# Performance work log

Measured on AMD Instinct MI355X. Metric: run time of the kernel, lower is better.

## Reference

```python
import jax, jax.numpy as jnp
import numpy as np

MEM_DIM = 128
ORDER = 256
THETA = 256.0
BATCH = 16
SEQ = 256
IN_DIM = 128


def _lmu_discrete_AB(order, theta):
    # Legendre delay network matrices (same construction as GenerateABMatrix)
    Q = np.arange(order, dtype=np.float64)
    R = (2.0 * Q + 1.0)[:, None]
    j, i = np.meshgrid(Q, Q)
    A = np.where(i < j, -1.0, (-1.0) ** (i - j + 1)) * R          # (O, O)
    B = ((-1.0) ** Q[:, None]) * R                                 # (O, 1)
    At = A.T / theta                                               # transposed system
    Bt = B.T / theta                                               # (1, O)
    # ZOH discretization on the transposed system: expm of padded block matrix
    em = np.concatenate([np.concatenate([At, Bt], axis=0),
                         np.zeros((order + 1, 1))], axis=1)        # (O+1, O+1)
    ms = jax.scipy.linalg.expm(jnp.asarray(em, jnp.float32))
    Ad = ms[:order, :order]                                        # (O, O)
    Bd = ms[order:, :order]                                        # (1, O)
    return Ad, Bd


def setup_inputs() -> dict:
    key = jax.random.key(0)
    kx, kw = jax.random.split(key)
    x = jax.random.normal(kx, (BATCH, SEQ, IN_DIM), dtype=jnp.float32)
    # glorot-uniform MemoryKernel (inputDim, MemoryDim)
    limit = np.sqrt(6.0 / (IN_DIM + MEM_DIM))
    memory_kernel = jax.random.uniform(kw, (IN_DIM, MEM_DIM), dtype=jnp.float32,
                                       minval=-limit, maxval=limit)
    A, B_mat = _lmu_discrete_AB(ORDER, THETA)
    return {"x": x, "memory_kernel": memory_kernel, "A": A, "B_mat": B_mat}


def reference(x, memory_kernel, A, B_mat):
    """LRMUCell (hiddenCell=None, no memory/hidden feedback) unrolled over SEQ.

    Per step: u_t = x_t @ K ; m_t = m_{t-1} @ Ad + u_t[:, :, None] * Bd
    Returns the final flattened memory state (batch, MemoryDim * Order).
    """
    Bsz, T, D = x.shape
    M = memory_kernel.shape[1]
    O = A.shape[0]
    # No feedback into u, so the input projection can be hoisted out of the scan.
    u_all = jnp.einsum('btd,dm->tbm', x, memory_kernel)  # (T, B, M)

    def step(m, u):
        # m: (B, M, O); u: (B, M)
        # (B,M,1) @ (1,O) is an outer product along the last axes
        m_new = jnp.matmul(m, A) + u[..., None] * B_mat
        return m_new, None

    m0 = jnp.zeros((Bsz, M, O), dtype=x.dtype)
    m_final, _ = jax.lax.scan(step, m0, u_all)
    return m_final.reshape(Bsz, M * O)
```

## Files before the change

### kernel.cpp

```cpp
#include <hip/hip_runtime.h>


#define SEQ_T 256
#define DIM 128
#define ORD 256
#define BMROWS 2048
#define NCHAIN 64

#define OFF_U 0
#define OFF_P (SEQ_T * BMROWS)
#define OFF_A0 (OFF_P + ORD * ORD)
#define OFF_A1 (OFF_A0 + ORD * ORD)
#define OFF_FLAGS (OFF_A1 + ORD * ORD)

#define LD_A(p) \
  __hip_atomic_load((p), __ATOMIC_RELAXED, __HIP_MEMORY_SCOPE_AGENT)
#define ST_A(p, v) \
  __hip_atomic_store((p), (v), __ATOMIC_RELAXED, __HIP_MEMORY_SCOPE_AGENT)

__device__ __forceinline__ void chain_bar(unsigned* flags, unsigned target) {
  __syncthreads();
  asm volatile("s_waitcnt vmcnt(0)" ::: "memory");
  const int t = threadIdx.x;
  if (t < NCHAIN) {
    if (t == (int)blockIdx.x) ST_A(&flags[t * 16], target);
    while (LD_A(&flags[t * 16]) < target) __builtin_amdgcn_s_sleep(2);
  }
  __syncthreads();
}

__global__ __launch_bounds__(256) void lrmu_main(
    const float* __restrict__ x, const float* __restrict__ K,
    const float* __restrict__ A, const float* __restrict__ Bm,
    float* __restrict__ ws) {
  __shared__ __align__(16) float ls[6 * ORD];
  __shared__ __align__(16) float red[4 * 6 * ORD];
  float* U = ws + OFF_U;
  float* P = ws + OFF_P;
  float* A0 = ws + OFF_A0;
  float* A1 = ws + OFF_A1;
  unsigned* flags = (unsigned*)(ws + OFF_FLAGS);
  const int blk = blockIdx.x, tid = threadIdx.x;

  if (blk >= NCHAIN) {
    float* xs = red;
    for (int u = blk - NCHAIN; u < 256; u += 256 - NCHAIN) {
      int b = u >> 4, tc = u & 15;
      for (int idx = tid; idx < 16 * DIM; idx += 256)
        xs[idx] = x[(b * SEQ_T + tc * 16) * DIM + idx];
      __syncthreads();
      int m = tid & 127, th = tid >> 7;
      float acc[8] = {};
#pragma unroll 8
      for (int d = 0; d < DIM; ++d) {
        float kv = K[d * DIM + m];
#pragma unroll
        for (int r = 0; r < 8; ++r)
          acc[r] = fmaf(xs[(th * 8 + r) * DIM + d], kv, acc[r]);
      }
#pragma unroll
      for (int r = 0; r < 8; ++r)
        U[(tc * 16 + th * 8 + r) * BMROWS + b * DIM + m] = acc[r];
      __syncthreads();
    }
    return;
  }

  const int lane = tid & 63, q = tid >> 6;
  for (int k = 0; k < 8; ++k) {
    const float* S = (k == 0) ? A : ((k & 1) ? A0 : A1);
    float* Snew = (k & 1) ? A1 : A0;
    const int half = 1 << k;
    const int nsr = (k < 7) ? 4 : 0;
    const int ndr = (k == 7) ? 2 : (blk < half ? 1 : 0);
    const int tr = nsr + ndr;

#pragma unroll
    for (int j = 0; j < 6; ++j) {
      int e = tid + 256 * j;
      int s = e >> 8, c = e & 255;
      float v = 0.f;
      if (s < nsr) {
        v = LD_A((float*)&S[(4 * blk + s) * ORD + c]);
      } else if (s - nsr < ndr) {
        int d = blk + 64 * (s - nsr);
        v = (k == 0) ? Bm[c] : LD_A(&P[d * ORD + c]);
      }
      ls[e] = v;
    }
    if (k == 0 && blk == 0) ST_A(&P[tid], Bm[tid]);
    __syncthreads();

    float acc[6][4];
#pragma unroll
    for (int s = 0; s < 6; ++s)
#pragma unroll
      for (int j = 0; j < 4; ++j) acc[s][j] = 0.f;
#pragma unroll 4
    for (int ii = 0; ii < 64; ++ii) {
      int i = (q << 6) + ii;
      float sv0 = LD_A((float*)&S[i * ORD + lane]);
      float sv1 = LD_A((float*)&S[i * ORD + lane + 64]);
      float sv2 = LD_A((float*)&S[i * ORD + lane + 128]);
      float sv3 = LD_A((float*)&S[i * ORD + lane + 192]);
#pragma unroll
      for (int s = 0; s < 6; ++s) {
        float lv = ls[s * ORD + i];
        acc[s][0] = fmaf(lv, sv0, acc[s][0]);
        acc[s][1] = fmaf(lv, sv1, acc[s][1]);
        acc[s][2] = fmaf(lv, sv2, acc[s][2]);
        acc[s][3] = fmaf(lv, sv3, acc[s][3]);
      }
    }
#pragma unroll
    for (int s = 0; s < 6; ++s)
#pragma unroll
      for (int j = 0; j < 4; ++j)
        red[(q * 6 + s) * ORD + (j << 6) + lane] = acc[s][j];
    __syncthreads();

#pragma unroll
    for (int j = 0; j < 6; ++j) {
      int o = tid + 256 * j;
      int s = o >> 8, c = o & 255;
      if (s < tr) {
        float sum = red[o] + red[1536 + o] + red[3072 + o] + red[4608 + o];
        float* dst;
        if (s < nsr) {
          dst = &Snew[(4 * blk + s) * ORD + c];
        } else {
          int d = blk + 64 * (s - nsr);
          dst = &P[(half + d) * ORD + c];
        }
        ST_A(dst, sum);
      }
    }
    if (k < 7) chain_bar(flags, (unsigned)(k + 1));
  }
}

__global__ __launch_bounds__(256) void lrmu_out(
    const float* __restrict__ U, const float* __restrict__ P,
    float* __restrict__ out) {
  __shared__ __align__(16) float us[SEQ_T * 8];
  int bm0 = blockIdx.x * 8;
  int tid = threadIdx.x;
  for (int idx = tid; idx < SEQ_T * 8; idx += 256) {
    int t = idx >> 3, r = idx & 7;
    us[idx] = U[t * BMROWS + bm0 + r];
  }
  __syncthreads();
  float acc[8] = {};
  int c = tid;
#pragma unroll 8
  for (int t = 0; t < SEQ_T; ++t) {
    float pv = P[(SEQ_T - 1 - t) * ORD + c];
    const float4 u0 = *(const float4*)&us[t * 8];
    const float4 u1 = *(const float4*)&us[t * 8 + 4];
    acc[0] = fmaf(u0.x, pv, acc[0]);
    acc[1] = fmaf(u0.y, pv, acc[1]);
    acc[2] = fmaf(u0.z, pv, acc[2]);
    acc[3] = fmaf(u0.w, pv, acc[3]);
    acc[4] = fmaf(u1.x, pv, acc[4]);
    acc[5] = fmaf(u1.y, pv, acc[5]);
    acc[6] = fmaf(u1.z, pv, acc[6]);
    acc[7] = fmaf(u1.w, pv, acc[7]);
  }
#pragma unroll
  for (int r = 0; r < 8; ++r) out[(bm0 + r) * ORD + c] = acc[r];
}

extern "C" void kernel_launch(void* const* d_in, const int* in_sizes, int n_in,
                              void* d_out, int out_size, void* d_ws,
                              size_t ws_size, hipStream_t stream) {
  const float* x = (const float*)d_in[0];
  const float* K = (const float*)d_in[1];
  const float* A = (const float*)d_in[2];
  const float* Bm = (const float*)d_in[3];
  float* out = (float*)d_out;
  float* ws = (float*)d_ws;

  hipMemsetAsync(ws + OFF_FLAGS, 0, 4096, stream);
  lrmu_main<<<256, 256, 0, stream>>>(x, K, A, Bm, ws);
  lrmu_out<<<BMROWS / 8, 256, 0, stream>>>(ws + OFF_U, ws + OFF_P, out);
}
```

Before: 143.5 us.

## Fuse projection, squaring chain and output into one persistent kernel

Merges the projection, the matrix-power doubling chain and the output contraction into a single 256-block kernel that uses grid-wide flag barriers. The chain work is now split over all 256 blocks as 64 row groups by 4 column groups, with the S column tile staged in LDS and partial sums reduced by shuffles. Each squaring step writes to its own buffer, so there are no read/write hazards across steps. The intent is to remove a kernel launch and spread the serial chain over four times as many CUs, at the cost of a barrier across all 256 blocks that spins without sleeping and assumes every block is co-resident.

Result: no change. 144.0 us (+0.4%).

```diff
diff --git a/kernel.cpp b/kernel.cpp
--- a/kernel.cpp
+++ b/kernel.cpp
@@ -5,169 +5,172 @@
 #define DIM 128
 #define ORD 256
 #define BMROWS 2048
-#define NCHAIN 64
 
 #define OFF_U 0
-#define OFF_P (SEQ_T * BMROWS)
-#define OFF_A0 (OFF_P + ORD * ORD)
-#define OFF_A1 (OFF_A0 + ORD * ORD)
-#define OFF_FLAGS (OFF_A1 + ORD * ORD)
+#define OFF_P (OFF_U + SEQ_T * BMROWS)
+#define APSTRIDE (ORD * ORD + 2048)
+#define OFF_AP (OFF_P + ORD * ORD + 2048)
+#define OFF_FLAGS (OFF_AP + 7 * APSTRIDE + 2048)
 
 #define LD_A(p) \
   __hip_atomic_load((p), __ATOMIC_RELAXED, __HIP_MEMORY_SCOPE_AGENT)
 #define ST_A(p, v) \
   __hip_atomic_store((p), (v), __ATOMIC_RELAXED, __HIP_MEMORY_SCOPE_AGENT)
 
-__device__ __forceinline__ void chain_bar(unsigned* flags, unsigned target) {
+__device__ __forceinline__ void gbar(unsigned* flags, unsigned target) {
+  asm volatile("s_waitcnt vmcnt(0)" ::: "memory");
   __syncthreads();
-  asm volatile("s_waitcnt vmcnt(0)" ::: "memory");
-  const int t = threadIdx.x;
-  if (t < NCHAIN) {
-    if (t == (int)blockIdx.x) ST_A(&flags[t * 16], target);
-    while (LD_A(&flags[t * 16]) < target) __builtin_amdgcn_s_sleep(2);
+  if ((int)threadIdx.x == (int)blockIdx.x) ST_A(&flags[threadIdx.x], target);
+  while (LD_A(&flags[threadIdx.x]) < target) {
   }
   __syncthreads();
 }
 
-__global__ __launch_bounds__(256) void lrmu_main(
+__global__ __launch_bounds__(256) void lrmu_all(
     const float* __restrict__ x, const float* __restrict__ K,
     const float* __restrict__ A, const float* __restrict__ Bm,
-    float* __restrict__ ws) {
-  __shared__ __align__(16) float ls[6 * ORD];
-  __shared__ __align__(16) float red[4 * 6 * ORD];
+    float* __restrict__ out, float* __restrict__ ws) {
+  __shared__ __align__(16) float Slds[ORD * 64];
+  __shared__ __align__(16) float lsb[2048];
+  __shared__ __align__(16) float redb[4 * 320];
   float* U = ws + OFF_U;
   float* P = ws + OFF_P;
-  float* A0 = ws + OFF_A0;
-  float* A1 = ws + OFF_A1;
   unsigned* flags = (unsigned*)(ws + OFF_FLAGS);
   const int blk = blockIdx.x, tid = threadIdx.x;
 
-  if (blk >= NCHAIN) {
-    float* xs = red;
-    for (int u = blk - NCHAIN; u < 256; u += 256 - NCHAIN) {
-      int b = u >> 4, tc = u & 15;
-      for (int idx = tid; idx < 16 * DIM; idx += 256)
-        xs[idx] = x[(b * SEQ_T + tc * 16) * DIM + idx];
-      __syncthreads();
-      int m = tid & 127, th = tid >> 7;
-      float acc[8] = {};
+  {
+    int b = blk >> 4, tc = blk & 15;
+    float* xs = Slds;
+    for (int idx = tid; idx < 16 * DIM; idx += 256)
+      xs[idx] = x[(b * SEQ_T + tc * 16) * DIM + idx];
+    __syncthreads();
+    int m = tid & 127, th = tid >> 7;
+    float acc[8] = {};
 #pragma unroll 8
-      for (int d = 0; d < DIM; ++d) {
-        float kv = K[d * DIM + m];
-#pragma unroll
-        for (int r = 0; r < 8; ++r)
-          acc[r] = fmaf(xs[(th * 8 + r) * DIM + d], kv, acc[r]);
-      }
+    for (int d = 0; d < DIM; ++d) {
+      float kv = K[d * DIM + m];
 #pragma unroll
       for (int r = 0; r < 8; ++r)
-        U[(tc * 16 + th * 8 + r) * BMROWS + b * DIM + m] = acc[r];
-      __syncthreads();
+        acc[r] = fmaf(xs[(th * 8 + r) * DIM + d], kv, acc[r]);
     }
-    return;
+#pragma unroll
+    for (int r = 0; r < 8; ++r)
+      ST_A(&U[(tc * 16 + th * 8 + r) * BMROWS + b * DIM + m], acc[r]);
+    if (blk == 0) ST_A(&P[tid], Bm[tid]);
+    __syncthreads();
   }
 
+  const int rg = blk >> 2, cg = blk & 3;
   const int lane = tid & 63, q = tid >> 6;
+  const int ir = lane >> 4, c4 = (lane & 15) * 4;
   for (int k = 0; k < 8; ++k) {
-    const float* S = (k == 0) ? A : ((k & 1) ? A0 : A1);
-    float* Snew = (k & 1) ? A1 : A0;
+    const float* S = (k == 0) ? A : (ws + OFF_AP + (k - 1) * APSTRIDE);
+    float* Snew = ws + OFF_AP + ((k < 7) ? k : 6) * APSTRIDE;
     const int half = 1 << k;
-    const int nsr = (k < 7) ? 4 : 0;
-    const int ndr = (k == 7) ? 2 : (blk < half ? 1 : 0);
-    const int tr = nsr + ndr;
+    const int nsq = (k < 7) ? 4 : 0;
+    const int ndb = (k == 7) ? 2 : (rg < half ? 1 : 0);
+    const int nrows = nsq + ndb;
 
 #pragma unroll
-    for (int j = 0; j < 6; ++j) {
-      int e = tid + 256 * j;
-      int s = e >> 8, c = e & 255;
+    for (int s = 0; s < 5; ++s) {
       float v = 0.f;
-      if (s < nsr) {
-        v = LD_A((float*)&S[(4 * blk + s) * ORD + c]);
-      } else if (s - nsr < ndr) {
-        int d = blk + 64 * (s - nsr);
-        v = (k == 0) ? Bm[c] : LD_A(&P[d * ORD + c]);
+      if (s < nsq) {
+        v = S[(4 * rg + s) * ORD + tid];
+      } else if (s - nsq < ndb) {
+        int d = rg + 64 * (s - nsq);
+        v = (k == 0) ? Bm[tid] : P[d * ORD + tid];
       }
-      ls[e] = v;
+      lsb[s * ORD + tid] = v;
     }
-    if (k == 0 && blk == 0) ST_A(&P[tid], Bm[tid]);
+#pragma unroll
+    for (int j = 0; j < 16; ++j) {
+      int f = tid + 256 * j;
+      int i = f >> 4, cc = (f & 15) * 4;
+      *(float4*)&Slds[i * 64 + cc] =
+          *(const float4*)&S[i * ORD + cg * 64 + cc];
+    }
     __syncthreads();
 
-    float acc[6][4];
+    float acc[5][4] = {};
+#pragma unroll 4
+    for (int ii = 0; ii < 16; ++ii) {
+      int i = q * 64 + 4 * ii + ir;
+      float4 sv = *(const float4*)&Slds[i * 64 + c4];
 #pragma unroll
-    for (int s = 0; s < 6; ++s)
-#pragma unroll
-      for (int j = 0; j < 4; ++j) acc[s][j] = 0.f;
-#pragma unroll 4
-    for (int ii = 0; ii < 64; ++ii) {
-      int i = (q << 6) + ii;
-      float sv0 = LD_A((float*)&S[i * ORD + lane]);
-      float sv1 = LD_A((float*)&S[i * ORD + lane + 64]);
-      float sv2 = LD_A((float*)&S[i * ORD + lane + 128]);
-      float sv3 = LD_A((float*)&S[i * ORD + lane + 192]);
-#pragma unroll
-      for (int s = 0; s < 6; ++s) {
-        float lv = ls[s * ORD + i];
-        acc[s][0] = fmaf(lv, sv0, acc[s][0]);
-        acc[s][1] = fmaf(lv, sv1, acc[s][1]);
-        acc[s][2] = fmaf(lv, sv2, acc[s][2]);
-        acc[s][3] = fmaf(lv, sv3, acc[s][3]);
+      for (int s = 0; s < 5; ++s) {
+        float lv = lsb[s * ORD + i];
+        acc[s][0] = fmaf(lv, sv.x, acc[s][0]);
+        acc[s][1] = fmaf(lv, sv.y, acc[s][1]);
+        acc[s][2] = fmaf(lv, sv.z, acc[s][2]);
+        acc[s][3] = fmaf(lv, sv.w, acc[s][3]);
       }
     }
 #pragma unroll
-    for (int s = 0; s < 6; ++s)
+    for (int s = 0; s < 5; ++s)
 #pragma unroll
-      for (int j = 0; j < 4; ++j)
-        red[(q * 6 + s) * ORD + (j << 6) + lane] = acc[s][j];
+      for (int w = 0; w < 4; ++w) {
+        acc[s][w] += __shfl_xor(acc[s][w], 16);
+        acc[s][w] += __shfl_xor(acc[s][w], 32);
+      }
+    if (ir == 0) {
+#pragma unroll
+      for (int s = 0; s < 5; ++s)
+        *(float4*)&redb[q * 320 + s * 64 + c4] =
+            make_float4(acc[s][0], acc[s][1], acc[s][2], acc[s][3]);
+    }
     __syncthreads();
-
-#pragma unroll
-    for (int j = 0; j < 6; ++j) {
-      int o = tid + 256 * j;
-      int s = o >> 8, c = o & 255;
-      if (s < tr) {
-        float sum = red[o] + red[1536 + o] + red[3072 + o] + red[4608 + o];
-        float* dst;
-        if (s < nsr) {
-          dst = &Snew[(4 * blk + s) * ORD + c];
+    for (int o = tid; o < 320; o += 256) {
+      int s = o >> 6, c = o & 63;
+      if (s < nrows) {
+        float sum = redb[o] + redb[320 + o] + redb[640 + o] + redb[960 + o];
+        if (s < nsq) {
+          ST_A(&Snew[(4 * rg + s) * ORD + cg * 64 + c], sum);
         } else {
-          int d = blk + 64 * (s - nsr);
-          dst = &P[(half + d) * ORD + c];
+          int d = rg + 64 * (s - nsq);
+          ST_A(&P[(half + d) * ORD + cg * 64 + c], sum);
         }
-        ST_A(dst, sum);
       }
     }
-    if (k < 7) chain_bar(flags, (unsigned)(k + 1));
+    gbar(flags, (unsigned)(k + 1));
   }
-}
 
-__global__ __launch_bounds__(256) void lrmu_out(
-    const float* __restrict__ U, const float* __restrict__ P,
-    float* __restrict__ out) {
-  __shared__ __align__(16) float us[SEQ_T * 8];
-  int bm0 = blockIdx.x * 8;
-  int tid = threadIdx.x;
-  for (int idx = tid; idx < SEQ_T * 8; idx += 256) {
-    int t = idx >> 3, r = idx & 7;
-    us[idx] = U[t * BMROWS + bm0 + r];
+  {
+    float* us = lsb;
+    float* redo = Slds;
+    int bm0 = blk * 8;
+    for (int idx = tid; idx < SEQ_T * 8; idx += 256) {
+      int t = idx >> 3, r = idx & 7;
+      us[idx] = U[t * BMROWS + bm0 + r];
+    }
+    __syncthreads();
+    int c4o = lane * 4, qo = q;
+    float ao[8][4] = {};
+#pragma unroll 4
+    for (int tt = 0; tt < 64; ++tt) {
+      int t = qo * 64 + tt;
+      float4 pv = *(const float4*)&P[(SEQ_T - 1 - t) * ORD + c4o];
+      float4 u0 = *(const float4*)&us[t * 8];
+      float4 u1 = *(const float4*)&us[t * 8 + 4];
+      float uv[8] = {u0.x, u0.y, u0.z, u0.w, u1.x, u1.y, u1.z, u1.w};
+      float pw[4] = {pv.x, pv.y, pv.z, pv.w};
+#pragma unroll
+      for (int r = 0; r < 8; ++r)
+#pragma unroll
+        for (int w = 0; w < 4; ++w)
+          ao[r][w] = fmaf(uv[r], pw[w], ao[r][w]);
+    }
+#pragma unroll
+    for (int r = 0; r < 8; ++r)
+      *(float4*)&redo[qo * 2048 + r * 256 + c4o] =
+          make_float4(ao[r][0], ao[r][1], ao[r][2], ao[r][3]);
+    __syncthreads();
+#pragma unroll
+    for (int j = 0; j < 8; ++j) {
+      int o = tid + 256 * j;
+      float s = redo[o] + redo[2048 + o] + redo[4096 + o] + redo[6144 + o];
+      out[bm0 * ORD + o] = s;
+    }
   }
-  __syncthreads();
-  float acc[8] = {};
-  int c = tid;
-#pragma unroll 8
-  for (int t = 0; t < SEQ_T; ++t) {
-    float pv = P[(SEQ_T - 1 - t) * ORD + c];
-    const float4 u0 = *(const float4*)&us[t * 8];
-    const float4 u1 = *(const float4*)&us[t * 8 + 4];
-    acc[0] = fmaf(u0.x, pv, acc[0]);
-    acc[1] = fmaf(u0.y, pv, acc[1]);
-    acc[2] = fmaf(u0.z, pv, acc[2]);
-    acc[3] = fmaf(u0.w, pv, acc[3]);
-    acc[4] = fmaf(u1.x, pv, acc[4]);
-    acc[5] = fmaf(u1.y, pv, acc[5]);
-    acc[6] = fmaf(u1.z, pv, acc[6]);
-    acc[7] = fmaf(u1.w, pv, acc[7]);
-  }
-#pragma unroll
-  for (int r = 0; r < 8; ++r) out[(bm0 + r) * ORD + c] = acc[r];
 }
 
 extern "C" void kernel_launch(void* const* d_in, const int* in_sizes, int n_in,
@@ -180,7 +183,6 @@
   float* out = (float*)d_out;
   float* ws = (float*)d_ws;
 
-  hipMemsetAsync(ws + OFF_FLAGS, 0, 4096, stream);
-  lrmu_main<<<256, 256, 0, stream>>>(x, K, A, Bm, ws);
-  lrmu_out<<<BMROWS / 8, 256, 0, stream>>>(ws + OFF_U, ws + OFF_P, out);
+  hipMemsetAsync(ws + OFF_FLAGS, 0, 256 * sizeof(unsigned), stream);
+  lrmu_all<<<256, 256, 0, stream>>>(x, K, A, Bm, out, ws);
 }
```
